# Kernel optimization log

Hardware: AMD Instinct MI355X
Metric: run time of the kernel (lower is better)

The kernel has to match this reference:

```python
import jax, jax.numpy as jnp
import numpy as np

B, S, I, H = 512, 1024, 20, 64  # batch, seq_len, input_size, hidden_size


def setup_inputs() -> dict:
    key = jax.random.key(0)
    ks = jax.random.split(key, 12)
    # one-hot protein sequences with variable true lengths (padding is all-zero rows)
    lengths = jax.random.randint(ks[0], (B,), 100, S + 1)
    tokens = jax.random.randint(ks[1], (B, S), 0, I)
    valid = (jnp.arange(S)[None, :] < lengths[:, None]).astype(jnp.float32)
    input1 = jax.nn.one_hot(tokens, I, dtype=jnp.float32) * valid[:, :, None]

    def nrm(k, shape, s=0.05):
        return jax.random.normal(k, shape, jnp.float32) * s

    return {
        'input1': input1,
        'W_ih_f': nrm(ks[2], (4 * H, I)), 'W_hh_f': nrm(ks[3], (4 * H, H)), 'b_f': nrm(ks[4], (4 * H,)),
        'W_ih_b': nrm(ks[5], (4 * H, I)), 'W_hh_b': nrm(ks[6], (4 * H, H)), 'b_b': nrm(ks[7], (4 * H,)),
        'conv1_w': nrm(ks[8], (20, 20), 1.0),           # blosum pssm: [out_c=20, kernel_w=20]
        'conv2_w': nrm(ks[9], (100, 4, 20)), 'conv2_b': nrm(ks[9], (100,)),
        'fc1_w': nrm(ks[10], (64, 228)), 'fc1_b': nrm(ks[10], (64,)),
        'fc2_w': nrm(ks[11], (2, 64)), 'fc2_b': nrm(ks[11], (2,)),
    }


def _lstm_final(x, W_ih, W_hh, b):
    # x: [B,S,I] -> final hidden state [B,H]; torch gate order i,f,g,o
    xs = jnp.einsum('bsi,gi->sbg', x, W_ih) + b  # [S,B,4H]

    def step(carry, gx):
        h, c = carry
        g = gx + h @ W_hh.T
        i, f, gg, o = jnp.split(g, 4, axis=-1)
        c = jax.nn.sigmoid(f) * c + jax.nn.sigmoid(i) * jnp.tanh(gg)
        h = jax.nn.sigmoid(o) * jnp.tanh(c)
        return (h, c), None

    init = (jnp.zeros((x.shape[0], H), x.dtype), jnp.zeros((x.shape[0], H), x.dtype))
    (h, _), _ = jax.lax.scan(step, init, xs)
    return h


def reference(input1, W_ih_f, W_hh_f, b_f, W_ih_b, W_hh_b, b_b,
              conv1_w, conv2_w, conv2_b, fc1_w, fc1_b, fc2_w, fc2_b):
    # BiLSTM: final hidden state of each direction (dropout is identity in eval)
    h_fw = _lstm_final(input1, W_ih_f, W_hh_f, b_f)
    h_bw = _lstm_final(input1[:, ::-1, :], W_ih_b, W_hh_b, b_b)
    lstm_output = jnp.concatenate([h_fw, h_bw], axis=1)  # [B,128]

    # conv1: kernel (1,20) spans the full width -> per-position linear map. [B,20,S]
    c1 = jnp.einsum('bsj,cj->bcs', input1, conv1_w)
    # faithful torch.reshape (B,20,S,1)->(B,S,1,20): row-major reinterpretation
    c1 = c1.reshape(input1.shape[0], S, 20)  # [B,S,20]

    # ragged 4-bin segment mean over the first width[i]=4*(len[i]//4) positions
    lens = jnp.sum(input1, axis=(1, 2)).astype(jnp.int32)
    bw = jnp.floor(lens / 4).astype(jnp.int32)
    width = bw * 4
    pos = jnp.arange(S)[None, :]                       # [1,S]
    bin_idx = pos // bw[:, None]                       # [B,S]
    valid = pos < width[:, None]                       # [B,S]
    mask = ((bin_idx[:, None, :] == jnp.arange(4)[None, :, None]) & valid[:, None, :]).astype(c1.dtype)  # [B,4,S]
    avblock = jnp.einsum('bks,bsc->bkc', mask, c1) / bw.astype(c1.dtype)[:, None, None]  # [B,4,20]

    # conv2: kernel (4,20) spans the whole avblock -> one dot per out channel
    c2 = jnp.einsum('bkc,okc->bo', avblock, conv2_w) + conv2_b  # [B,100]
    c2 = jax.nn.relu(c2)

    merged = jnp.concatenate([lstm_output, c2], axis=1)  # [B,228]
    fc1 = merged @ fc1_w.T + fc1_b
    fc2 = fc1 @ fc2_w.T + fc2_b
    return jax.nn.softmax(fc2, axis=1)
```

## Files before the change

### kernel.cpp

```cpp
#include <hip/hip_runtime.h>
#include <hip/hip_bf16.h>

#define BB 512
#define SS 1024
#define NI 20
#define HH 64
#define NG 256
#define MB4 4
#define PAD 80
#define TSTR 257

typedef unsigned short u16;
typedef unsigned int u32;
typedef unsigned long long u64;
typedef _Float16 f16;
typedef f16 f16x8 __attribute__((ext_vector_type(8)));
typedef float f32x4 __attribute__((ext_vector_type(4)));

#define LOG2E 1.4426950408889634f

__device__ __forceinline__ float bf2f(u16 b) { return __uint_as_float(((u32)b) << 16); }
__device__ __forceinline__ float ldw(const void* p, int idx, int mode) {
  return mode ? bf2f(((const u16*)p)[idx]) : ((const float*)p)[idx];
}
__device__ __forceinline__ float frcp(float x) { return __builtin_amdgcn_rcpf(x); }
__device__ __forceinline__ float fexp2(float x) { return __builtin_amdgcn_exp2f(x); }

__global__ __launch_bounds__(256)
void lstm_kernel(const void* in1,
                 const void* Wih_f, const void* Whh_f, const void* b_f,
                 const void* Wih_b, const void* Whh_b, const void* b_b,
                 short* toks_g, int* lens, float* hout) {
  int bx = blockIdx.x;
  int dir = bx >> 7;
  int b0 = (bx & 127) * MB4;
  int t = threadIdx.x;
  int w = t >> 6, lane = t & 63, l = lane & 15, q = lane >> 4;
  int bsel = l >> 2;

  __shared__ __align__(16) float table[21 * TSTR];
  __shared__ __align__(16) f16 hbuf[2][MB4][PAD];
  __shared__ short tok_s[SS * MB4];
  __shared__ u64 red[256];
  __shared__ int mode_sh;

  if (t == 0) mode_sh = 1;
  __syncthreads();
  {
    float v = bf2f(((const u16*)b_f)[t]);
    if (!(fabsf(v) < 1000.0f)) atomicAnd(&mode_sh, 0);
  }
  __syncthreads();
  int mode = mode_sh;
  const void* Wih = dir ? Wih_b : Wih_f;
  const void* Whh = dir ? Whh_b : Whh_f;
  const void* bv  = dir ? b_b   : b_f;

  u64 cnt = 0;
  for (int m = 0; m < MB4; ++m) {
    if (mode) {
      u32* st = (u32*)table;
      for (int k0 = 0; k0 < 4; ++k0) {
        const u32* src = (const u32*)in1 + ((size_t)(b0 + m) * SS + k0 * 256) * 10;
#pragma unroll
        for (int i = 0; i < 10; ++i) st[t + i * 256] = src[t + i * 256];
        __syncthreads();
        const u32* row = st + t * 10;
        int tok = -1;
#pragma unroll
        for (int ww = 0; ww < 10; ++ww) {
          u32 u = row[ww];
          if (u & 0xFFFFu) tok = 2 * ww;
          if (u >> 16)     tok = 2 * ww + 1;
        }
        tok_s[(k0 * 256 + t) * MB4 + m] = (short)(tok + 1);
        if (dir == 0) toks_g[(size_t)(b0 + m) * SS + k0 * 256 + t] = (short)tok;
        cnt += (u64)(tok >= 0) << (16 * m);
        __syncthreads();
      }
    } else {
      float4* st = (float4*)table;
      for (int k0 = 0; k0 < 4; ++k0) {
        const float4* src = (const float4*)((const float*)in1 + ((size_t)(b0 + m) * SS + k0 * 256) * 20);
#pragma unroll
        for (int i = 0; i < 5; ++i) st[t + i * 256] = src[t + i * 256];
        __syncthreads();
        const float* row = (const float*)table + t * 20;
        int tok = -1;
#pragma unroll
        for (int ww = 0; ww < 20; ++ww)
          if (row[ww] != 0.f) tok = ww;
        tok_s[(k0 * 256 + t) * MB4 + m] = (short)(tok + 1);
        if (dir == 0) toks_g[(size_t)(b0 + m) * SS + k0 * 256 + t] = (short)tok;
        cnt += (u64)(tok >= 0) << (16 * m);
        __syncthreads();
      }
    }
  }
  red[t] = cnt;
  __syncthreads();
  for (int stp = 128; stp > 0; stp >>= 1) {
    if (t < stp) red[t] += red[t + stp];
    __syncthreads();
  }
  if (dir == 0 && t < MB4)
    lens[b0 + t] = (int)((red[0] >> (16 * t)) & 0xFFFFull);
  __syncthreads();

  for (int idx = t; idx < 21 * 256; idx += 256) {
    int r = idx >> 8, g = idx & 255;
    float scl = ((g >> 6) == 2) ? (2.f * LOG2E) : (-LOG2E);
    float v = ldw(bv, g, mode);
    if (r > 0) v += ldw(Wih, g * NI + (r - 1), mode);
    table[r * TSTR + g] = scl * v;
  }
  f16x8 Bf[4][2];
#pragma unroll
  for (int tt = 0; tt < 4; ++tt) {
    float scl = (tt == 2) ? (2.f * LOG2E) : (-LOG2E);
    int g = 64 * tt + 16 * w + l;
#pragma unroll
    for (int kc = 0; kc < 2; ++kc) {
      f16x8 v;
#pragma unroll
      for (int j = 0; j < 8; ++j)
        v[j] = (f16)(scl * ldw(Whh, g * HH + kc * 32 + q * 8 + j, mode));
      Bf[tt][kc] = v;
    }
  }
  for (int idx = t; idx < 2 * MB4 * PAD; idx += 256)
    ((f16*)hbuf)[idx] = (f16)0.f;
  __syncthreads();

  float c_st = 0.f, hlast = 0.f;
  int jj = 16 * w + l;
  int tbase = 16 * w + l;

  float wxc[4];
  {
    int pos0 = dir ? (SS - 1) : 0;
    int base = (int)tok_s[pos0 * MB4 + q] * TSTR + tbase;
    wxc[0] = table[base];       wxc[1] = table[base + 64];
    wxc[2] = table[base + 128]; wxc[3] = table[base + 192];
  }
  int tok1;
  {
    int pos1 = dir ? (SS - 2) : 1;
    tok1 = (int)tok_s[pos1 * MB4 + q];
  }

#pragma unroll 2
  for (int s = 0; s < SS; ++s) {
    int p = s & 1;
    f16x8 a0 = *(const f16x8*)&hbuf[p][bsel][q * 8];
    f16x8 a1 = *(const f16x8*)&hbuf[p][bsel][32 + q * 8];
    float wxn[4];
    {
      int base = tok1 * TSTR + tbase;
      wxn[0] = table[base];       wxn[1] = table[base + 64];
      wxn[2] = table[base + 128]; wxn[3] = table[base + 192];
    }
    {
      int pos2 = (dir ? (SS - 3 - s) : (s + 2)) & (SS - 1);
      tok1 = (int)tok_s[pos2 * MB4 + q];
    }

    f32x4 acc[4];
#pragma unroll
    for (int tt = 0; tt < 4; ++tt) {
      f32x4 ci = {wxc[tt], wxc[tt], wxc[tt], wxc[tt]};
      acc[tt] = __builtin_amdgcn_mfma_f32_16x16x32_f16(a0, Bf[tt][0], ci, 0, 0, 0);
    }
#pragma unroll
    for (int tt = 0; tt < 4; ++tt)
      acc[tt] = __builtin_amdgcn_mfma_f32_16x16x32_f16(a1, Bf[tt][1], acc[tt], 0, 0, 0);

    {
      float Ei = fexp2(acc[0][0]);
      float Ef = fexp2(acc[1][0]);
      float G  = fexp2(acc[2][0]);
      float Eo = fexp2(acc[3][0]);
      float Ei1 = Ei + 1.f, Ef1 = Ef + 1.f, G1 = G + 1.f, Gm = G - 1.f;
      float t1 = Ei1 * G1;
      float num = fmaf(c_st, t1, Gm * Ef1);
      float cv = num * frcp(t1 * Ef1);
      c_st = cv;
      float C = fexp2((2.f * LOG2E) * cv);
      float hv = (C - 1.f) * frcp((Eo + 1.f) * (C + 1.f));
      hlast = hv;
      hbuf[p ^ 1][q][jj] = (f16)hv;
    }
    __syncthreads();
    wxc[0] = wxn[0]; wxc[1] = wxn[1]; wxc[2] = wxn[2]; wxc[3] = wxn[3];
  }
  hout[(b0 + q) * 128 + dir * 64 + jj] = hlast;
}

__global__ __launch_bounds__(256)
void head_kernel(const void* conv1_w, const void* conv2_w, const void* conv2_b,
                 const void* fc1_w, const void* fc1_b,
                 const void* fc2_w, const void* fc2_b,
                 const void* bvec, const short* toks, const int* lens,
                 const float* hout, void* out) {
  int t = threadIdx.x;
  __shared__ float c1w[400];
  __shared__ float c2w[100 * 80];
  __shared__ float f1w[64 * 228];
  __shared__ float f2w[128];
  __shared__ short tok_s[SS];
  __shared__ float pav[2][80];
  __shared__ float avg[80];
  __shared__ float merged[228];
  __shared__ float fpart[4][64];
  __shared__ float fc1v[64];
  __shared__ int mode_sh;

  if (t == 0) mode_sh = 1;
  __syncthreads();
  {
    float v = bf2f(((const u16*)bvec)[t]);
    if (!(fabsf(v) < 1000.0f)) atomicAnd(&mode_sh, 0);
  }
  __syncthreads();
  int mode = mode_sh;

  for (int i = t; i < 400; i += 256) c1w[i] = ldw(conv1_w, i, mode);
  for (int i = t; i < 100 * 80; i += 256) c2w[i] = ldw(conv2_w, i, mode);
  for (int i = t; i < 64 * 228; i += 256) f1w[i] = ldw(fc1_w, i, mode);
  if (t < 128) f2w[t] = ldw(fc2_w, t, mode);

  for (int pb = 0; pb < 2; ++pb) {
    int b = blockIdx.x * 2 + pb;
    __syncthreads();
    for (int s = t; s < SS; s += 256) tok_s[s] = toks[(size_t)b * SS + s];
    __syncthreads();

    int len = lens[b];
    int bw = len >> 2;
    if (t < 160) {
      int half = t / 80;
      int u = t - half * 80;
      int k = u / 20, cc = u % 20;
      int start = k * bw, mid = k * bw + (bw >> 1), end = (k + 1) * bw;
      int s0 = half ? mid : start;
      int s1 = half ? end : mid;
      float sum = 0.f;
      for (int s = s0; s < s1; ++s) {
        int f = s * 20 + cc;
        int ch = f >> 10;
        int pos = f & 1023;
        int tk = tok_s[pos];
        if (tk >= 0) sum += c1w[ch * 20 + tk];
      }
      pav[half][u] = sum;
    }
    __syncthreads();
    if (t < 80) avg[t] = (pav[0][t] + pav[1][t]) / (float)bw;
    __syncthreads();

    if (t < 128) merged[t] = hout[b * 128 + t];
    if (t >= 128 && t < 228) {
      int o = t - 128;
      float dot = ldw(conv2_b, o, mode);
#pragma unroll
      for (int q = 0; q < 80; ++q)
        dot += avg[q] * c2w[o * 80 + q];
      merged[t] = dot > 0.f ? dot : 0.f;
    }
    __syncthreads();

    {
      int o = t & 63, ch = t >> 6;
      float v = 0.f;
      int m0 = ch * 57, m1 = m0 + 57;
      for (int m = m0; m < m1; ++m)
        v += merged[m] * f1w[o * 228 + m];
      fpart[ch][o] = v;
    }
    __syncthreads();
    if (t < 64)
      fc1v[t] = fpart[0][t] + fpart[1][t] + fpart[2][t] + fpart[3][t] + ldw(fc1_b, t, mode);
    __syncthreads();

    if (t < 128) {
      int o = t >> 6, m = t & 63;
      fpart[o][m] = fc1v[m] * f2w[o * 64 + m];
    }
    __syncthreads();
    for (int stp = 32; stp > 0; stp >>= 1) {
      if (t < 128) {
        int o = t >> 6, m = t & 63;
        if (m < stp) fpart[o][m] += fpart[o][m + stp];
      }
      __syncthreads();
    }
    if (t == 0) {
      float x0 = fpart[0][0] + ldw(fc2_b, 0, mode);
      float x1 = fpart[1][0] + ldw(fc2_b, 1, mode);
      float mx = fmaxf(x0, x1);
      float e0 = fexp2(LOG2E * (x0 - mx)), e1 = fexp2(LOG2E * (x1 - mx));
      float inv = 1.f / (e0 + e1);
      if (mode) {
        ((__hip_bfloat16*)out)[b * 2 + 0] = __float2bfloat16(e0 * inv);
        ((__hip_bfloat16*)out)[b * 2 + 1] = __float2bfloat16(e1 * inv);
      } else {
        ((float*)out)[b * 2 + 0] = e0 * inv;
        ((float*)out)[b * 2 + 1] = e1 * inv;
      }
    }
  }
}

extern "C" void kernel_launch(void* const* d_in, const int* in_sizes, int n_in,
                              void* d_out, int out_size, void* d_ws, size_t ws_size,
                              hipStream_t stream) {
  (void)in_sizes; (void)n_in; (void)out_size; (void)ws_size;
  char* ws = (char*)d_ws;
  int*   lens = (int*)(ws + 256);
  short* toks = (short*)(ws + 256 + 2048);
  float* hout = (float*)(ws + 256 + 2048 + (size_t)BB * SS * sizeof(short));

  lstm_kernel<<<256, 256, 0, stream>>>(d_in[0],
                                       d_in[1], d_in[2], d_in[3],
                                       d_in[4], d_in[5], d_in[6],
                                       toks, lens, hout);
  head_kernel<<<256, 256, 0, stream>>>(d_in[7], d_in[8], d_in[9],
                                       d_in[10], d_in[11], d_in[12], d_in[13],
                                       d_in[3], toks, lens, hout, d_out);
}
```

Baseline: 422.5 us.

## Restructure head kernel to one batch per block, drop shared weight staging

The head kernel now runs one batch row per block over 512 blocks instead of two rows per block over 256 blocks. It no longer copies the conv2 and fc weights (about 90 KB) into shared memory and reads them straight from global/L2. The ragged segment sum is split three ways across 240 threads with a 4-way unrolled accumulation, and conv2 is split across 200 threads. The aim is to cut the large shared-memory weight staging and raise occupancy, at the cost of repeated global weight reads per block.

```diff
diff --git a/kernel.cpp b/kernel.cpp
--- a/kernel.cpp
+++ b/kernel.cpp
@@ -202,17 +202,17 @@
                  const void* fc2_w, const void* fc2_b,
                  const void* bvec, const short* toks, const int* lens,
                  const float* hout, void* out) {
+  int b = blockIdx.x;
   int t = threadIdx.x;
   __shared__ float c1w[400];
-  __shared__ float c2w[100 * 80];
-  __shared__ float f1w[64 * 228];
-  __shared__ float f2w[128];
   __shared__ short tok_s[SS];
-  __shared__ float pav[2][80];
+  __shared__ float pav[3][80];
   __shared__ float avg[80];
+  __shared__ float cpart[2][100];
   __shared__ float merged[228];
   __shared__ float fpart[4][64];
   __shared__ float fc1v[64];
+  __shared__ float f2p[2][64];
   __shared__ int mode_sh;
 
   if (t == 0) mode_sh = 1;
@@ -225,88 +225,97 @@
   int mode = mode_sh;
 
   for (int i = t; i < 400; i += 256) c1w[i] = ldw(conv1_w, i, mode);
-  for (int i = t; i < 100 * 80; i += 256) c2w[i] = ldw(conv2_w, i, mode);
-  for (int i = t; i < 64 * 228; i += 256) f1w[i] = ldw(fc1_w, i, mode);
-  if (t < 128) f2w[t] = ldw(fc2_w, t, mode);
-
-  for (int pb = 0; pb < 2; ++pb) {
-    int b = blockIdx.x * 2 + pb;
-    __syncthreads();
-    for (int s = t; s < SS; s += 256) tok_s[s] = toks[(size_t)b * SS + s];
-    __syncthreads();
-
-    int len = lens[b];
-    int bw = len >> 2;
-    if (t < 160) {
-      int half = t / 80;
-      int u = t - half * 80;
-      int k = u / 20, cc = u % 20;
-      int start = k * bw, mid = k * bw + (bw >> 1), end = (k + 1) * bw;
-      int s0 = half ? mid : start;
-      int s1 = half ? end : mid;
-      float sum = 0.f;
-      for (int s = s0; s < s1; ++s) {
-        int f = s * 20 + cc;
-        int ch = f >> 10;
-        int pos = f & 1023;
-        int tk = tok_s[pos];
-        if (tk >= 0) sum += c1w[ch * 20 + tk];
-      }
-      pav[half][u] = sum;
-    }
-    __syncthreads();
-    if (t < 80) avg[t] = (pav[0][t] + pav[1][t]) / (float)bw;
-    __syncthreads();
-
-    if (t < 128) merged[t] = hout[b * 128 + t];
-    if (t >= 128 && t < 228) {
-      int o = t - 128;
-      float dot = ldw(conv2_b, o, mode);
-#pragma unroll
-      for (int q = 0; q < 80; ++q)
-        dot += avg[q] * c2w[o * 80 + q];
-      merged[t] = dot > 0.f ? dot : 0.f;
-    }
-    __syncthreads();
-
-    {
-      int o = t & 63, ch = t >> 6;
-      float v = 0.f;
-      int m0 = ch * 57, m1 = m0 + 57;
-      for (int m = m0; m < m1; ++m)
-        v += merged[m] * f1w[o * 228 + m];
-      fpart[ch][o] = v;
-    }
-    __syncthreads();
-    if (t < 64)
-      fc1v[t] = fpart[0][t] + fpart[1][t] + fpart[2][t] + fpart[3][t] + ldw(fc1_b, t, mode);
-    __syncthreads();
-
+  for (int s = t; s < SS; s += 256) tok_s[s] = toks[(size_t)b * SS + s];
+  __syncthreads();
+
+  int len = lens[b];
+  int bw = len >> 2;
+  if (t < 240) {
+    int seg = t / 80;
+    int u = t - seg * 80;
+    int k = u / 20, cc = u % 20;
+    int base = k * bw;
+    int s0 = base + (seg * bw) / 3;
+    int s1 = base + ((seg + 1) * bw) / 3;
+    float p0 = 0.f, p1 = 0.f, p2 = 0.f, p3 = 0.f;
+    int s = s0;
+    for (; s + 4 <= s1; s += 4) {
+      int f0 = s * 20 + cc, f1 = f0 + 20, f2 = f0 + 40, f3 = f0 + 60;
+      int tk0 = tok_s[f0 & 1023];
+      int tk1 = tok_s[f1 & 1023];
+      int tk2 = tok_s[f2 & 1023];
+      int tk3 = tok_s[f3 & 1023];
+      if (tk0 >= 0) p0 += c1w[(f0 >> 10) * 20 + tk0];
+      if (tk1 >= 0) p1 += c1w[(f1 >> 10) * 20 + tk1];
+      if (tk2 >= 0) p2 += c1w[(f2 >> 10) * 20 + tk2];
+      if (tk3 >= 0) p3 += c1w[(f3 >> 10) * 20 + tk3];
+    }
+    for (; s < s1; ++s) {
+      int f = s * 20 + cc;
+      int tk = tok_s[f & 1023];
+      if (tk >= 0) p0 += c1w[(f >> 10) * 20 + tk];
+    }
+    pav[seg][u] = (p0 + p1) + (p2 + p3);
+  }
+  __syncthreads();
+  if (t < 80) avg[t] = (pav[0][t] + pav[1][t] + pav[2][t]) / (float)bw;
+  __syncthreads();
+
+  if (t < 200) {
+    int half = t / 100, o = t - half * 100;
+    float dot = 0.f;
+    int q0 = half * 40;
+#pragma unroll 8
+    for (int q = q0; q < q0 + 40; ++q)
+      dot = fmaf(avg[q], ldw(conv2_w, o * 80 + q, mode), dot);
+    cpart[half][o] = dot;
+  }
+  if (t < 128) merged[t] = hout[b * 128 + t];
+  __syncthreads();
+  if (t < 100) {
+    float dot = cpart[0][t] + cpart[1][t] + ldw(conv2_b, t, mode);
+    merged[128 + t] = dot > 0.f ? dot : 0.f;
+  }
+  __syncthreads();
+
+  {
+    int o = t & 63, ch = t >> 6;
+    float v = 0.f;
+    int m0 = ch * 57;
+#pragma unroll 8
+    for (int m = m0; m < m0 + 57; ++m)
+      v = fmaf(merged[m], ldw(fc1_w, o * 228 + m, mode), v);
+    fpart[ch][o] = v;
+  }
+  __syncthreads();
+  if (t < 64)
+    fc1v[t] = fpart[0][t] + fpart[1][t] + fpart[2][t] + fpart[3][t] + ldw(fc1_b, t, mode);
+  __syncthreads();
+
+  if (t < 128) {
+    int o = t >> 6, m = t & 63;
+    f2p[o][m] = fc1v[m] * ldw(fc2_w, o * 64 + m, mode);
+  }
+  __syncthreads();
+  for (int stp = 32; stp > 0; stp >>= 1) {
     if (t < 128) {
       int o = t >> 6, m = t & 63;
-      fpart[o][m] = fc1v[m] * f2w[o * 64 + m];
+      if (m < stp) f2p[o][m] += f2p[o][m + stp];
     }
     __syncthreads();
-    for (int stp = 32; stp > 0; stp >>= 1) {
-      if (t < 128) {
-        int o = t >> 6, m = t & 63;
-        if (m < stp) fpart[o][m] += fpart[o][m + stp];
-      }
-      __syncthreads();
-    }
-    if (t == 0) {
-      float x0 = fpart[0][0] + ldw(fc2_b, 0, mode);
-      float x1 = fpart[1][0] + ldw(fc2_b, 1, mode);
-      float mx = fmaxf(x0, x1);
-      float e0 = fexp2(LOG2E * (x0 - mx)), e1 = fexp2(LOG2E * (x1 - mx));
-      float inv = 1.f / (e0 + e1);
-      if (mode) {
-        ((__hip_bfloat16*)out)[b * 2 + 0] = __float2bfloat16(e0 * inv);
-        ((__hip_bfloat16*)out)[b * 2 + 1] = __float2bfloat16(e1 * inv);
-      } else {
-        ((float*)out)[b * 2 + 0] = e0 * inv;
-        ((float*)out)[b * 2 + 1] = e1 * inv;
-      }
+  }
+  if (t == 0) {
+    float x0 = f2p[0][0] + ldw(fc2_b, 0, mode);
+    float x1 = f2p[1][0] + ldw(fc2_b, 1, mode);
+    float mx = fmaxf(x0, x1);
+    float e0 = fexp2(LOG2E * (x0 - mx)), e1 = fexp2(LOG2E * (x1 - mx));
+    float inv = frcp(e0 + e1);
+    if (mode) {
+      ((__hip_bfloat16*)out)[b * 2 + 0] = __float2bfloat16(e0 * inv);
+      ((__hip_bfloat16*)out)[b * 2 + 1] = __float2bfloat16(e1 * inv);
+    } else {
+      ((float*)out)[b * 2 + 0] = e0 * inv;
+      ((float*)out)[b * 2 + 1] = e1 * inv;
     }
   }
 }
@@ -324,7 +333,7 @@
                                        d_in[1], d_in[2], d_in[3],
                                        d_in[4], d_in[5], d_in[6],
                                        toks, lens, hout);
-  head_kernel<<<256, 256, 0, stream>>>(d_in[7], d_in[8], d_in[9],
-                                       d_in[10], d_in[11], d_in[12], d_in[13],
-                                       d_in[3], toks, lens, hout, d_out);
+  head_kernel<<<BB, 256, 0, stream>>>(d_in[7], d_in[8], d_in[9],
+                                      d_in[10], d_in[11], d_in[12], d_in[13],
+                                      d_in[3], toks, lens, hout, d_out);
 }
```

Result: faster. 390.1 us (-7.7%).
